# Performance work log

Hardware: AMD Instinct MI355X
Metric: run time of the kernel (lower is better)

Reference implementation:

```python
import jax, jax.numpy as jnp
from jax import lax
import numpy as np

B, T, F, H = 512, 256, 128, 256


def setup_inputs() -> dict:
    key = jax.random.key(0)
    ks = jax.random.split(key, 9)
    s = 0.05
    return {
        "X": jax.random.normal(ks[0], (B, T, F), dtype=jnp.float32),
        "attn1_W": jax.random.normal(ks[1], (T + 1, 2 * H + F), dtype=jnp.float32) * s,
        "attn1_b": jax.random.normal(ks[2], (T + 1,), dtype=jnp.float32) * s,
        "attn2_W": jax.random.normal(ks[3], (F, T + 1), dtype=jnp.float32) * s,
        "attn2_b": jax.random.normal(ks[4], (F,), dtype=jnp.float32) * s,
        "W_ih": jax.random.normal(ks[5], (4 * H, F), dtype=jnp.float32) * s,
        "W_hh": jax.random.normal(ks[6], (4 * H, H), dtype=jnp.float32) * s,
        "b_ih": jax.random.normal(ks[7], (4 * H,), dtype=jnp.float32) * s,
        "b_hh": jax.random.normal(ks[8], (4 * H,), dtype=jnp.float32) * s,
    }


def reference(X, attn1_W, attn1_b, attn2_W, attn2_b, W_ih, W_hh, b_ih, b_hh):
    b, t, f = X.shape
    h_dim = W_hh.shape[1]

    def step(carry, x_t):
        h, c = carry
        # input attention: concat [x, h, c] -> tanh(linear) -> linear -> gate x
        z = jnp.concatenate([x_t, h, c], axis=1)  # [B, F+2H]
        a = jnp.tanh(z @ attn1_W.T + attn1_b)      # [B, T+1]
        xi = (a @ attn2_W.T + attn2_b) * x_t       # [B, F]
        # LSTMCell (PyTorch gate order: i, f, g, o)
        gates = xi @ W_ih.T + b_ih + h @ W_hh.T + b_hh  # [B, 4H]
        i_g, f_g, g_g, o_g = jnp.split(gates, 4, axis=1)
        i_g = jax.nn.sigmoid(i_g)
        f_g = jax.nn.sigmoid(f_g)
        g_g = jnp.tanh(g_g)
        o_g = jax.nn.sigmoid(o_g)
        c_new = f_g * c + i_g * g_g
        h_new = o_g * jnp.tanh(c_new)
        return (h_new, c_new), (h_new, c_new)

    h0 = jnp.zeros((b, h_dim), dtype=X.dtype)
    c0 = jnp.zeros((b, h_dim), dtype=X.dtype)
    _, (hs, cs) = lax.scan(step, (h0, c0), jnp.swapaxes(X, 0, 1))  # [T,B,H]
    return jnp.swapaxes(hs, 0, 1), jnp.swapaxes(cs, 0, 1)  # [B,T,H]
```

## Files before the change

kernel.cpp:

```cpp
#include <hip/hip_runtime.h>


#define Bb 512
#define Tt 256
#define Ff 128
#define Hh 256

typedef unsigned short ushort_t;
typedef short s16x8 __attribute__((ext_vector_type(8)));
typedef float f32x4 __attribute__((ext_vector_type(4)));

#define A1_NK 20
#define A2_NK 9
#define IH_NK 4
#define HH_NK 8
#define CH_A1 0
#define CH_A2 21760
#define CH_IH 26368
#define CH_HH 42752
#define CH_TOTAL 75520

#define ZP 648
#define AP 296
#define XIP 136

__device__ inline ushort_t f2b(float f) {
    unsigned u = __float_as_uint(f);
    unsigned r = (u + 0x7fffu + ((u >> 16) & 1u)) >> 16;
    return (ushort_t)r;
}
__device__ inline float b2f(ushort_t u) {
    return __uint_as_float(((unsigned)u) << 16);
}
__device__ inline float fast_sig(float x) { return 1.f / (1.f + __expf(-x)); }
__device__ inline float fast_tanh(float x) {
    float cx = fminf(fmaxf(x, -15.f), 15.f);
    float e = __expf(2.f * cx);
    return (e - 1.f) / (e + 1.f);
}

__global__ void conv_kernel(const float* __restrict__ a1,
                            const float* __restrict__ a2,
                            const float* __restrict__ ih,
                            const float* __restrict__ hh,
                            ushort_t* __restrict__ ws) {
    int idx = blockIdx.x * 256 + threadIdx.x;
    if (idx >= CH_TOTAL) return;
    int lane = idx & 63;
    int jo = lane & 15;
    int ko = (lane >> 4) * 8;
    float v[8];
    if (idx < CH_A2) {
        int cix = idx >> 6;
        int tile = cix / A1_NK, kc = cix % A1_NK;
        int j = tile * 16 + jo, k = kc * 32 + ko;
        #pragma unroll
        for (int e = 0; e < 8; ++e) v[e] = (j < 257) ? a1[j * 640 + k + e] : 0.f;
    } else if (idx < CH_IH) {
        int cix = (idx - CH_A2) >> 6;
        int tile = cix / A2_NK, kc = cix % A2_NK;
        int j = tile * 16 + jo, k = kc * 32 + ko;
        #pragma unroll
        for (int e = 0; e < 8; ++e) v[e] = (k + e < 257) ? a2[j * 257 + k + e] : 0.f;
    } else if (idx < CH_HH) {
        int cix = (idx - CH_IH) >> 6;
        int tile = cix / IH_NK, kc = cix % IH_NK;
        int j = tile * 16 + jo, k = kc * 32 + ko;
        #pragma unroll
        for (int e = 0; e < 8; ++e) v[e] = ih[j * 128 + k + e];
    } else {
        int cix = (idx - CH_HH) >> 6;
        int tile = cix / HH_NK, kc = cix % HH_NK;
        int j = tile * 16 + jo, k = kc * 32 + ko;
        #pragma unroll
        for (int e = 0; e < 8; ++e) v[e] = hh[j * 256 + k + e];
    }
    union { s16x8 v8; ushort_t u[8]; } o;
    #pragma unroll
    for (int e = 0; e < 8; ++e) o.u[e] = f2b(v[e]);
    ((s16x8*)ws)[idx] = o.v8;
}

__global__ __launch_bounds__(512, 1) void lstm_mfma(
    const float* __restrict__ X,
    const float* __restrict__ b1,
    const float* __restrict__ b2,
    const float* __restrict__ bih,
    const float* __restrict__ bhh,
    const ushort_t* __restrict__ wsw,
    float* __restrict__ out)
{
    __shared__ s16x8    a2w[8 * A2_NK * 64];
    __shared__ ushort_t z_bf[16][ZP];
    __shared__ ushort_t a_bf[16][AP];
    __shared__ ushort_t xi_bf[16][XIP];

    const int tid = threadIdx.x;
    const int w   = tid >> 6;
    const int l   = tid & 63;
    const int lj  = l & 15;
    const int lr4 = (l >> 4) * 4;
    const int lk8 = (l >> 4) * 8;
    const int b0  = blockIdx.x * 16;

    const s16x8* __restrict__ W8 = (const s16x8*)wsw;

    float bgq[8];
    #pragma unroll
    for (int u = 0; u < 8; ++u) {
        int n = (u & 3) * 16 + (u >> 2) * 8 + w;
        int j = n * 16 + lj;
        bgq[u] = bih[j] + bhh[j];
    }

    for (int i = tid; i < 8 * A2_NK * 64; i += 512) a2w[i] = W8[CH_A2 + i];

    float bA1_0 = b1[16 * w + lj];
    float bA1_1 = b1[128 + 16 * w + lj];
    float b1_256 = (w == 0) ? b1[256] : 0.f;
    float bA2 = b2[16 * w + lj];

    f32x4 agate[8];
    float c_reg[8];
    #pragma unroll
    for (int u = 0; u < 8; ++u) c_reg[u] = 0.f;

    {
        s16x8 zz = {0, 0, 0, 0, 0, 0, 0, 0};
        #pragma unroll
        for (int rep = 0; rep < 2; ++rep) {
            int i = tid + rep * 512;
            int r = i >> 6, c = (i & 63) * 8;
            *(s16x8*)&z_bf[r][128 + c] = zz;
        }
        for (int i = tid; i < 592; i += 512) {
            int r = i / 37, c = (i - r * 37) * 8;
            *(s16x8*)&a_bf[r][c] = zz;
        }
    }
    if (tid < 256) {
        int r = tid >> 4, c = (tid & 15) * 8;
        float4 x0 = *(const float4*)&X[((size_t)(b0 + r) * Tt) * Ff + c];
        float4 x1 = *(const float4*)&X[((size_t)(b0 + r) * Tt) * Ff + c + 4];
        s16x8 v;
        v[0] = (short)f2b(x0.x); v[1] = (short)f2b(x0.y);
        v[2] = (short)f2b(x0.z); v[3] = (short)f2b(x0.w);
        v[4] = (short)f2b(x1.x); v[5] = (short)f2b(x1.y);
        v[6] = (short)f2b(x1.z); v[7] = (short)f2b(x1.w);
        *(s16x8*)&z_bf[r][c] = v;
    }
    __syncthreads();

    float* __restrict__ hs = out;
    float* __restrict__ cs = out + (size_t)Bb * Tt * Hh;

    float4 xp0, xp1;

    for (int t = 0; t < Tt; ++t) {
        {
            const s16x8* Wa = W8 + CH_A1;
            s16x8 bufA[5][2];
            #pragma unroll
            for (int kc = 0; kc < 4; ++kc) {
                bufA[kc][0] = Wa[(w * A1_NK + kc) * 64 + l];
                bufA[kc][1] = Wa[((8 + w) * A1_NK + kc) * 64 + l];
            }
            f32x4 acc0 = {0.f, 0.f, 0.f, 0.f};
            f32x4 acc1 = {0.f, 0.f, 0.f, 0.f};
            #pragma unroll
            for (int kc = 0; kc < A1_NK; ++kc) {
                if (kc + 4 < A1_NK) {
                    bufA[(kc + 4) % 5][0] = Wa[(w * A1_NK + kc + 4) * 64 + l];
                    bufA[(kc + 4) % 5][1] = Wa[((8 + w) * A1_NK + kc + 4) * 64 + l];
                }
                s16x8 a = *(const s16x8*)&z_bf[lj][kc * 32 + lk8];
                acc0 = __builtin_amdgcn_mfma_f32_16x16x32_bf16(a, bufA[kc % 5][0], acc0, 0, 0, 0);
                acc1 = __builtin_amdgcn_mfma_f32_16x16x32_bf16(a, bufA[kc % 5][1], acc1, 0, 0, 0);
            }
            int j0 = 16 * w + lj;
            #pragma unroll
            for (int q = 0; q < 4; ++q) {
                a_bf[lr4 + q][j0]       = f2b(fast_tanh(acc0[q] + bA1_0));
                a_bf[lr4 + q][128 + j0] = f2b(fast_tanh(acc1[q] + bA1_1));
            }
        }
        if (w == 0) {
            const s16x8* Wa = W8 + CH_A1 + 16 * A1_NK * 64;
            s16x8 buf16[4];
            #pragma unroll
            for (int kc = 0; kc < 3; ++kc) buf16[kc] = Wa[kc * 64 + l];
            f32x4 acc2 = {0.f, 0.f, 0.f, 0.f};
            #pragma unroll
            for (int kc = 0; kc < A1_NK; ++kc) {
                if (kc + 3 < A1_NK) buf16[(kc + 3) & 3] = Wa[(kc + 3) * 64 + l];
                s16x8 a = *(const s16x8*)&z_bf[lj][kc * 32 + lk8];
                acc2 = __builtin_amdgcn_mfma_f32_16x16x32_bf16(a, buf16[kc & 3], acc2, 0, 0, 0);
            }
            if (lj == 0) {
                #pragma unroll
                for (int q = 0; q < 4; ++q)
                    a_bf[lr4 + q][256] = f2b(fast_tanh(acc2[q] + b1_256));
            }
        }
        __syncthreads();

        if (tid < 256 && t + 1 < Tt) {
            const float* xs = &X[((size_t)(b0 + (tid >> 4)) * Tt + (t + 1)) * Ff + (tid & 15) * 8];
            xp0 = *(const float4*)xs;
            xp1 = *(const float4*)(xs + 4);
        }
        {
            s16x8 bufH[2][4];
            #pragma unroll
            for (int j2 = 0; j2 < 4; ++j2) {
                int n = (j2 & 3) * 16 + 0 * 8 + w;
                bufH[0][j2] = W8[CH_HH + (n * HH_NK + 0) * 64 + l];
            }
            #pragma unroll
            for (int u = 0; u < 8; ++u)
                agate[u] = (f32x4){bgq[u], bgq[u], bgq[u], bgq[u]};

            {
                f32x4 acc = {0.f, 0.f, 0.f, 0.f};
                #pragma unroll
                for (int kc = 0; kc < A2_NK; ++kc) {
                    s16x8 a = *(const s16x8*)&a_bf[lj][kc * 32 + lk8];
                    s16x8 b = a2w[(w * A2_NK + kc) * 64 + l];
                    acc = __builtin_amdgcn_mfma_f32_16x16x32_bf16(a, b, acc, 0, 0, 0);
                }
                int j = 16 * w + lj;
                #pragma unroll
                for (int q = 0; q < 4; ++q) {
                    int r = lr4 + q;
                    float xi = (acc[q] + bA2) * b2f(z_bf[r][j]);
                    xi_bf[r][j] = f2b(xi);
                }
            }

            s16x8 ah;
            #pragma unroll
            for (int g = 0; g < 16; ++g) {
                const int kc = g >> 1, half = g & 1;
                if (g + 1 < 16) {
                    const int kn = (g + 1) >> 1, hn = (g + 1) & 1;
                    #pragma unroll
                    for (int j2 = 0; j2 < 4; ++j2) {
                        int u = hn * 4 + j2;
                        int n = (u & 3) * 16 + (u >> 2) * 8 + w;
                        bufH[(g + 1) & 1][j2] = W8[CH_HH + (n * HH_NK + kn) * 64 + l];
                    }
                }
                if (half == 0)
                    ah = *(const s16x8*)&z_bf[lj][128 + kc * 32 + lk8];
                #pragma unroll
                for (int j2 = 0; j2 < 4; ++j2) {
                    int u = half * 4 + j2;
                    agate[u] = __builtin_amdgcn_mfma_f32_16x16x32_bf16(ah, bufH[g & 1][j2], agate[u], 0, 0, 0);
                }
            }
        }

        s16x8 bufI[2][4];
        #pragma unroll
        for (int j2 = 0; j2 < 4; ++j2) {
            int n = (j2 & 3) * 16 + 0 * 8 + w;
            bufI[0][j2] = W8[CH_IH + (n * IH_NK + 0) * 64 + l];
        }
        __syncthreads();

        {
            s16x8 ax;
            #pragma unroll
            for (int g = 0; g < 8; ++g) {
                const int kc = g >> 1, half = g & 1;
                if (g + 1 < 8) {
                    const int kn = (g + 1) >> 1, hn = (g + 1) & 1;
                    #pragma unroll
                    for (int j2 = 0; j2 < 4; ++j2) {
                        int u = hn * 4 + j2;
                        int n = (u & 3) * 16 + (u >> 2) * 8 + w;
                        bufI[(g + 1) & 1][j2] = W8[CH_IH + (n * IH_NK + kn) * 64 + l];
                    }
                }
                if (half == 0)
                    ax = *(const s16x8*)&xi_bf[lj][kc * 32 + lk8];
                #pragma unroll
                for (int j2 = 0; j2 < 4; ++j2) {
                    int u = half * 4 + j2;
                    agate[u] = __builtin_amdgcn_mfma_f32_16x16x32_bf16(ax, bufI[g & 1][j2], agate[u], 0, 0, 0);
                }
            }
            #pragma unroll
            for (int q = 0; q < 2; ++q) {
                int d = 128 * q + 16 * w + lj;
                #pragma unroll
                for (int qq = 0; qq < 4; ++qq) {
                    int r = lr4 + qq;
                    float gi = agate[q * 4 + 0][qq];
                    float gf = agate[q * 4 + 1][qq];
                    float gg = agate[q * 4 + 2][qq];
                    float go = agate[q * 4 + 3][qq];
                    float ig = fast_sig(gi);
                    float fg = fast_sig(gf);
                    float g_g = fast_tanh(gg);
                    float og = fast_sig(go);
                    float cn = fmaf(fg, c_reg[q * 4 + qq], ig * g_g);
                    float hn = og * fast_tanh(cn);
                    c_reg[q * 4 + qq] = cn;
                    z_bf[r][128 + d] = f2b(hn);
                    z_bf[r][384 + d] = f2b(cn);
                    size_t oi = ((size_t)(b0 + r) * Tt + t) * Hh + d;
                    hs[oi] = hn;
                    cs[oi] = cn;
                }
            }
        }
        if (tid < 256 && t + 1 < Tt) {
            int r = tid >> 4, c = (tid & 15) * 8;
            s16x8 v;
            v[0] = (short)f2b(xp0.x); v[1] = (short)f2b(xp0.y);
            v[2] = (short)f2b(xp0.z); v[3] = (short)f2b(xp0.w);
            v[4] = (short)f2b(xp1.x); v[5] = (short)f2b(xp1.y);
            v[6] = (short)f2b(xp1.z); v[7] = (short)f2b(xp1.w);
            *(s16x8*)&z_bf[r][c] = v;
        }
        __syncthreads();
    }
}

extern "C" void kernel_launch(void* const* d_in, const int* in_sizes, int n_in,
                              void* d_out, int out_size, void* d_ws, size_t ws_size,
                              hipStream_t stream) {
    const float* X   = (const float*)d_in[0];
    const float* a1W = (const float*)d_in[1];
    const float* a1b = (const float*)d_in[2];
    const float* a2W = (const float*)d_in[3];
    const float* a2b = (const float*)d_in[4];
    const float* Wih = (const float*)d_in[5];
    const float* Whh = (const float*)d_in[6];
    const float* bih = (const float*)d_in[7];
    const float* bhh = (const float*)d_in[8];
    ushort_t* ws = (ushort_t*)d_ws;

    hipLaunchKernelGGL(conv_kernel, dim3(CH_TOTAL / 256), dim3(256), 0, stream,
                       a1W, a2W, Wih, Whh, ws);
    hipLaunchKernelGGL(lstm_mfma, dim3(32), dim3(512), 0, stream,
                       X, a1b, a2b, bih, bhh, ws, (float*)d_out);
}
```

Measured before the change: 7.442 ms.

## Prefetch weights across stage barriers and replace serial attn column MFMA with wave reduction

The weight prefetch pipeline is deepened from double to triple buffering. The first weight chunks for the next stage are issued before each __syncthreads, so global loads overlap barriers and the tanh/activation epilogues. The 257th attention-1 output column, previously a 20-MFMA serial chain run only by wave 0, is now computed by every wave. Each wave handles two rows as a scalar dot product using a small LDS copy of that weight column and a shuffle reduction, removing the load imbalance. The trade-off is higher register pressure from the larger persistent buffers, which risks spills.

```diff
diff --git a/kernel.cpp b/kernel.cpp
--- a/kernel.cpp
+++ b/kernel.cpp
@@ -94,6 +94,7 @@
     __shared__ ushort_t z_bf[16][ZP];
     __shared__ ushort_t a_bf[16][AP];
     __shared__ ushort_t xi_bf[16][XIP];
+    __shared__ ushort_t w16[640];
 
     const int tid = threadIdx.x;
     const int w   = tid >> 6;
@@ -114,16 +115,24 @@
     }
 
     for (int i = tid; i < 8 * A2_NK * 64; i += 512) a2w[i] = W8[CH_A2 + i];
+    if (tid < 80) {
+        int kc = tid >> 2, sub = tid & 3;
+        *(s16x8*)&w16[kc * 32 + sub * 8] = W8[CH_A1 + (16 * A1_NK + kc) * 64 + sub * 16];
+    }
 
     float bA1_0 = b1[16 * w + lj];
     float bA1_1 = b1[128 + 16 * w + lj];
-    float b1_256 = (w == 0) ? b1[256] : 0.f;
-    float bA2 = b2[16 * w + lj];
+    float b256  = b1[256];
+    float bA2   = b2[16 * w + lj];
 
     f32x4 agate[8];
     float c_reg[8];
     #pragma unroll
     for (int u = 0; u < 8; ++u) c_reg[u] = 0.f;
+
+    s16x8 bufA[5][2];
+    s16x8 bufH[3][4];
+    s16x8 bufI[3][4];
 
     {
         s16x8 zz = {0, 0, 0, 0, 0, 0, 0, 0};
@@ -149,6 +158,12 @@
         v[6] = (short)f2b(x1.z); v[7] = (short)f2b(x1.w);
         *(s16x8*)&z_bf[r][c] = v;
     }
+
+    #pragma unroll
+    for (int kc = 0; kc < 5; ++kc) {
+        bufA[kc][0] = W8[CH_A1 + (w * A1_NK + kc) * 64 + l];
+        bufA[kc][1] = W8[CH_A1 + ((8 + w) * A1_NK + kc) * 64 + l];
+    }
     __syncthreads();
 
     float* __restrict__ hs = out;
@@ -159,23 +174,26 @@
     for (int t = 0; t < Tt; ++t) {
         {
             const s16x8* Wa = W8 + CH_A1;
-            s16x8 bufA[5][2];
-            #pragma unroll
-            for (int kc = 0; kc < 4; ++kc) {
-                bufA[kc][0] = Wa[(w * A1_NK + kc) * 64 + l];
-                bufA[kc][1] = Wa[((8 + w) * A1_NK + kc) * 64 + l];
-            }
             f32x4 acc0 = {0.f, 0.f, 0.f, 0.f};
             f32x4 acc1 = {0.f, 0.f, 0.f, 0.f};
             #pragma unroll
             for (int kc = 0; kc < A1_NK; ++kc) {
-                if (kc + 4 < A1_NK) {
-                    bufA[(kc + 4) % 5][0] = Wa[(w * A1_NK + kc + 4) * 64 + l];
-                    bufA[(kc + 4) % 5][1] = Wa[((8 + w) * A1_NK + kc + 4) * 64 + l];
-                }
                 s16x8 a = *(const s16x8*)&z_bf[lj][kc * 32 + lk8];
                 acc0 = __builtin_amdgcn_mfma_f32_16x16x32_bf16(a, bufA[kc % 5][0], acc0, 0, 0, 0);
                 acc1 = __builtin_amdgcn_mfma_f32_16x16x32_bf16(a, bufA[kc % 5][1], acc1, 0, 0, 0);
+                if (kc + 5 < A1_NK) {
+                    bufA[kc % 5][0] = Wa[(w * A1_NK + kc + 5) * 64 + l];
+                    bufA[kc % 5][1] = Wa[((8 + w) * A1_NK + kc + 5) * 64 + l];
+                }
+            }
+            #pragma unroll
+            for (int g = 0; g < 3; ++g) {
+                #pragma unroll
+                for (int j2 = 0; j2 < 4; ++j2) {
+                    int u = (g & 1) * 4 + j2;
+                    int n = (u & 3) * 16 + (u >> 2) * 8 + w;
+                    bufH[g][j2] = W8[CH_HH + (n * HH_NK + (g >> 1)) * 64 + l];
+                }
             }
             int j0 = 16 * w + lj;
             #pragma unroll
@@ -183,23 +201,24 @@
                 a_bf[lr4 + q][j0]       = f2b(fast_tanh(acc0[q] + bA1_0));
                 a_bf[lr4 + q][128 + j0] = f2b(fast_tanh(acc1[q] + bA1_1));
             }
-        }
-        if (w == 0) {
-            const s16x8* Wa = W8 + CH_A1 + 16 * A1_NK * 64;
-            s16x8 buf16[4];
-            #pragma unroll
-            for (int kc = 0; kc < 3; ++kc) buf16[kc] = Wa[kc * 64 + l];
-            f32x4 acc2 = {0.f, 0.f, 0.f, 0.f};
-            #pragma unroll
-            for (int kc = 0; kc < A1_NK; ++kc) {
-                if (kc + 3 < A1_NK) buf16[(kc + 3) & 3] = Wa[(kc + 3) * 64 + l];
-                s16x8 a = *(const s16x8*)&z_bf[lj][kc * 32 + lk8];
-                acc2 = __builtin_amdgcn_mfma_f32_16x16x32_bf16(a, buf16[kc & 3], acc2, 0, 0, 0);
-            }
-            if (lj == 0) {
-                #pragma unroll
-                for (int q = 0; q < 4; ++q)
-                    a_bf[lr4 + q][256] = f2b(fast_tanh(acc2[q] + b1_256));
+            {
+                int r0 = 2 * w, r1 = 2 * w + 1;
+                float d0 = 0.f, d1 = 0.f;
+                #pragma unroll
+                for (int jj = 0; jj < 10; ++jj) {
+                    float wv = b2f(w16[l + 64 * jj]);
+                    d0 = fmaf(b2f(z_bf[r0][l + 64 * jj]), wv, d0);
+                    d1 = fmaf(b2f(z_bf[r1][l + 64 * jj]), wv, d1);
+                }
+                #pragma unroll
+                for (int m = 1; m < 64; m <<= 1) {
+                    d0 += __shfl_xor(d0, m, 64);
+                    d1 += __shfl_xor(d1, m, 64);
+                }
+                if (l == 0) {
+                    a_bf[r0][256] = f2b(fast_tanh(d0 + b256));
+                    a_bf[r1][256] = f2b(fast_tanh(d1 + b256));
+                }
             }
         }
         __syncthreads();
@@ -209,62 +228,55 @@
             xp0 = *(const float4*)xs;
             xp1 = *(const float4*)(xs + 4);
         }
+        #pragma unroll
+        for (int u = 0; u < 8; ++u)
+            agate[u] = (f32x4){bgq[u], bgq[u], bgq[u], bgq[u]};
         {
-            s16x8 bufH[2][4];
-            #pragma unroll
-            for (int j2 = 0; j2 < 4; ++j2) {
-                int n = (j2 & 3) * 16 + 0 * 8 + w;
-                bufH[0][j2] = W8[CH_HH + (n * HH_NK + 0) * 64 + l];
-            }
-            #pragma unroll
-            for (int u = 0; u < 8; ++u)
-                agate[u] = (f32x4){bgq[u], bgq[u], bgq[u], bgq[u]};
-
-            {
-                f32x4 acc = {0.f, 0.f, 0.f, 0.f};
-                #pragma unroll
-                for (int kc = 0; kc < A2_NK; ++kc) {
-                    s16x8 a = *(const s16x8*)&a_bf[lj][kc * 32 + lk8];
-                    s16x8 b = a2w[(w * A2_NK + kc) * 64 + l];
-                    acc = __builtin_amdgcn_mfma_f32_16x16x32_bf16(a, b, acc, 0, 0, 0);
-                }
-                int j = 16 * w + lj;
-                #pragma unroll
-                for (int q = 0; q < 4; ++q) {
-                    int r = lr4 + q;
-                    float xi = (acc[q] + bA2) * b2f(z_bf[r][j]);
-                    xi_bf[r][j] = f2b(xi);
-                }
-            }
-
+            f32x4 acc = {0.f, 0.f, 0.f, 0.f};
+            #pragma unroll
+            for (int kc = 0; kc < A2_NK; ++kc) {
+                s16x8 a = *(const s16x8*)&a_bf[lj][kc * 32 + lk8];
+                s16x8 b = a2w[(w * A2_NK + kc) * 64 + l];
+                acc = __builtin_amdgcn_mfma_f32_16x16x32_bf16(a, b, acc, 0, 0, 0);
+            }
+            int j = 16 * w + lj;
+            #pragma unroll
+            for (int q = 0; q < 4; ++q) {
+                int r = lr4 + q;
+                float xi = (acc[q] + bA2) * b2f(z_bf[r][j]);
+                xi_bf[r][j] = f2b(xi);
+            }
+        }
+        {
             s16x8 ah;
             #pragma unroll
             for (int g = 0; g < 16; ++g) {
-                const int kc = g >> 1, half = g & 1;
-                if (g + 1 < 16) {
-                    const int kn = (g + 1) >> 1, hn = (g + 1) & 1;
+                const int kc = g >> 1, half = g & 1, slot = g % 3;
+                if (half == 0)
+                    ah = *(const s16x8*)&z_bf[lj][128 + kc * 32 + lk8];
+                #pragma unroll
+                for (int j2 = 0; j2 < 4; ++j2)
+                    agate[half * 4 + j2] = __builtin_amdgcn_mfma_f32_16x16x32_bf16(
+                        ah, bufH[slot][j2], agate[half * 4 + j2], 0, 0, 0);
+                if (g + 3 < 16) {
+                    const int gg = g + 3, kn = gg >> 1, hn = gg & 1;
                     #pragma unroll
                     for (int j2 = 0; j2 < 4; ++j2) {
                         int u = hn * 4 + j2;
                         int n = (u & 3) * 16 + (u >> 2) * 8 + w;
-                        bufH[(g + 1) & 1][j2] = W8[CH_HH + (n * HH_NK + kn) * 64 + l];
+                        bufH[slot][j2] = W8[CH_HH + (n * HH_NK + kn) * 64 + l];
                     }
                 }
-                if (half == 0)
-                    ah = *(const s16x8*)&z_bf[lj][128 + kc * 32 + lk8];
-                #pragma unroll
-                for (int j2 = 0; j2 < 4; ++j2) {
-                    int u = half * 4 + j2;
-                    agate[u] = __builtin_amdgcn_mfma_f32_16x16x32_bf16(ah, bufH[g & 1][j2], agate[u], 0, 0, 0);
-                }
-            }
-        }
-
-        s16x8 bufI[2][4];
-        #pragma unroll
-        for (int j2 = 0; j2 < 4; ++j2) {
-            int n = (j2 & 3) * 16 + 0 * 8 + w;
-            bufI[0][j2] = W8[CH_IH + (n * IH_NK + 0) * 64 + l];
+            }
+        }
+        #pragma unroll
+        for (int g = 0; g < 3; ++g) {
+            #pragma unroll
+            for (int j2 = 0; j2 < 4; ++j2) {
+                int u = (g & 1) * 4 + j2;
+                int n = (u & 3) * 16 + (u >> 2) * 8 + w;
+                bufI[g][j2] = W8[CH_IH + (n * IH_NK + (g >> 1)) * 64 + l];
+            }
         }
         __syncthreads();
 
@@ -272,22 +284,21 @@
             s16x8 ax;
             #pragma unroll
             for (int g = 0; g < 8; ++g) {
-                const int kc = g >> 1, half = g & 1;
-                if (g + 1 < 8) {
-                    const int kn = (g + 1) >> 1, hn = (g + 1) & 1;
+                const int kc = g >> 1, half = g & 1, slot = g % 3;
+                if (half == 0)
+                    ax = *(const s16x8*)&xi_bf[lj][kc * 32 + lk8];
+                #pragma unroll
+                for (int j2 = 0; j2 < 4; ++j2)
+                    agate[half * 4 + j2] = __builtin_amdgcn_mfma_f32_16x16x32_bf16(
+                        ax, bufI[slot][j2], agate[half * 4 + j2], 0, 0, 0);
+                if (g + 3 < 8) {
+                    const int gg = g + 3, kn = gg >> 1, hn = gg & 1;
                     #pragma unroll
                     for (int j2 = 0; j2 < 4; ++j2) {
                         int u = hn * 4 + j2;
                         int n = (u & 3) * 16 + (u >> 2) * 8 + w;
-                        bufI[(g + 1) & 1][j2] = W8[CH_IH + (n * IH_NK + kn) * 64 + l];
+                        bufI[slot][j2] = W8[CH_IH + (n * IH_NK + kn) * 64 + l];
                     }
-                }
-                if (half == 0)
-                    ax = *(const s16x8*)&xi_bf[lj][kc * 32 + lk8];
-                #pragma unroll
-                for (int j2 = 0; j2 < 4; ++j2) {
-                    int u = half * 4 + j2;
-                    agate[u] = __builtin_amdgcn_mfma_f32_16x16x32_bf16(ax, bufI[g & 1][j2], agate[u], 0, 0, 0);
                 }
             }
             #pragma unroll
@@ -324,6 +335,11 @@
             v[6] = (short)f2b(xp1.z); v[7] = (short)f2b(xp1.w);
             *(s16x8*)&z_bf[r][c] = v;
         }
+        #pragma unroll
+        for (int kc = 0; kc < 5; ++kc) {
+            bufA[kc][0] = W8[CH_A1 + (w * A1_NK + kc) * 64 + l];
+            bufA[kc][1] = W8[CH_A1 + ((8 + w) * A1_NK + kc) * 64 + l];
+        }
         __syncthreads();
     }
 }
```

Result: slower. 7.682 ms (+3.2%).
